# Performance work log

Hardware: AMD Instinct MI355X
Metric: run time of the kernel (lower is better)

Reference implementation:

```python
import jax, jax.numpy as jnp
import numpy as np

N, E = 4096, 4096          # nodes, hyperedges
IN_DIM, OUT_DIM, EDGE_DIM = 256, 256, 64
HEADS, DEG, CARD = 8, 8, 8  # node degree, edge cardinality (regular hypergraph)


def setup_inputs() -> dict:
    key = jax.random.key(0)
    ks = jax.random.split(key, 6)
    # regular hypergraph: DEG rounds, each a permutation of nodes chunked into
    # blocks of CARD -> every node in exactly DEG edges, every edge has CARD
    # distinct nodes. E = DEG * N / CARD.
    rng = np.random.default_rng(0)
    node_of_edge = np.concatenate(
        [rng.permutation(N).reshape(-1, CARD) for _ in range(DEG)], axis=0)  # [E, CARD]
    inc = np.zeros((E, N), dtype=np.float32)
    inc[np.arange(E)[:, None], node_of_edge] = 1.0
    s = 0.05
    return {
        "x": jax.random.normal(ks[0], (N, IN_DIM), jnp.float32),
        "incidence": jnp.asarray(inc),
        "edge_attr": jax.random.normal(ks[1], (E, EDGE_DIM), jnp.float32),
        "W_lin": jax.random.normal(ks[2], (IN_DIM, OUT_DIM), jnp.float32) * s,
        "W_edge": jax.random.normal(ks[3], (EDGE_DIM, OUT_DIM), jnp.float32) * s,
        "in_proj_w": jax.random.normal(ks[4], (3 * OUT_DIM, OUT_DIM), jnp.float32) * s,
        "in_proj_b": jnp.zeros((3 * OUT_DIM,), jnp.float32),
        "out_proj_w": jax.random.normal(ks[5], (OUT_DIM, OUT_DIM), jnp.float32) * s,
        "out_proj_b": jnp.zeros((OUT_DIM,), jnp.float32),
        "deg": DEG,
        "card": CARD,
    }


def reference(x, incidence, edge_attr, W_lin, W_edge,
              in_proj_w, in_proj_b, out_proj_w, out_proj_b, deg, card):
    n = x.shape[0]
    Wh = x @ W_lin          # [N, D]
    We = edge_attr @ W_edge  # [E, D]
    Dm = Wh.shape[1]
    H = HEADS
    dh = Dm // H
    # recover regular structure from the binary incidence matrix.
    # (attention is permutation-invariant over the pair set, so the order of
    #  indices returned by top_k vs torch.nonzero does not matter)
    _, edge_of_node = jax.lax.top_k(incidence.T, deg)   # [N, deg]
    _, node_of_edge = jax.lax.top_k(incidence, card)    # [E, card]
    pair_e = edge_of_node[:, :, None]                   # [N, deg, 1]
    pair_u = node_of_edge[edge_of_node]                 # [N, deg, card]
    L = deg * card
    Ksrc = (Wh[pair_u] + We[pair_e]).reshape(n, L, Dm)  # key source per pair
    Vsrc = Wh[pair_u].reshape(n, L, Dm)                 # value source per pair
    # torch nn.MultiheadAttention in/out projections
    Wq, Wk, Wv = jnp.split(in_proj_w, 3, axis=0)
    bq, bk, bv = jnp.split(in_proj_b, 3)
    q = (Wh @ Wq.T + bq).reshape(n, H, dh)              # q_len = 1 per node
    k = (Ksrc @ Wk.T + bk).reshape(n, L, H, dh)
    v = (Vsrc @ Wv.T + bv).reshape(n, L, H, dh)
    scale = 1.0 / jnp.sqrt(jnp.asarray(dh, q.dtype))
    scores = jnp.einsum('nhd,nlhd->nhl', q, k) * scale  # [N, H, L]
    attn = jax.nn.softmax(scores, axis=-1)
    ctx = jnp.einsum('nhl,nlhd->nhd', attn, v).reshape(n, Dm)
    out = ctx @ out_proj_w.T + out_proj_b
    return jax.nn.relu(out)
```

## Files before the change

kernel.cpp:

```cpp
#include <hip/hip_runtime.h>
#include <hip/hip_bf16.h>

#define NN    4096
#define EE    4096
#define DM    256
#define EDIM  64
#define HH    8
#define DHd   32
#define LL    64

typedef short  s16x8 __attribute__((ext_vector_type(8)));
typedef unsigned short u16x8 __attribute__((ext_vector_type(8)));
typedef float  f32x4 __attribute__((ext_vector_type(4)));

#define SCALE 0.17677669529663687f

__device__ __forceinline__ float b2f(unsigned short u) {
  return __uint_as_float(((unsigned int)u) << 16);
}
__device__ __forceinline__ unsigned short f2b_bits(float f) {
  unsigned int u = __float_as_uint(f);
  u = (u + 0x7FFFu + ((u >> 16) & 1u)) >> 16;
  return (unsigned short)u;
}

#define MODE_PLAIN 0
#define MODE_PROJ  1
#define MODE_OUT   2

__device__ __forceinline__ void gemm_mfma_body(
    short* As, short* Bs, f32x4 acc[2][2], int wr, int wc, int fr, int fk) {
  s16x8 af0 = *(const s16x8*)&As[(wr + fr) * 40 + fk];
  s16x8 af1 = *(const s16x8*)&As[(wr + 16 + fr) * 40 + fk];
  s16x8 bf0 = *(const s16x8*)&Bs[(wc + fr) * 40 + fk];
  s16x8 bf1 = *(const s16x8*)&Bs[(wc + 16 + fr) * 40 + fk];
  acc[0][0] = __builtin_amdgcn_mfma_f32_16x16x32_bf16(af0, bf0, acc[0][0], 0, 0, 0);
  acc[0][1] = __builtin_amdgcn_mfma_f32_16x16x32_bf16(af0, bf1, acc[0][1], 0, 0, 0);
  acc[1][0] = __builtin_amdgcn_mfma_f32_16x16x32_bf16(af1, bf0, acc[1][0], 0, 0, 0);
  acc[1][1] = __builtin_amdgcn_mfma_f32_16x16x32_bf16(af1, bf1, acc[1][1], 0, 0, 0);
}

__device__ __forceinline__ void gemm_tile(
    const unsigned short* __restrict__ A, const unsigned short* __restrict__ B,
    int i0, int j0, int N, int K, int mode,
    float* __restrict__ out_f, unsigned short* __restrict__ out_b,
    unsigned short* __restrict__ out_b2, const float* __restrict__ bias,
    short* As, short* Bs) {
  const int tid  = threadIdx.x;
  const int wid  = tid >> 6, lane = tid & 63;
  const int wr   = (wid >> 1) * 32, wc = (wid & 1) * 32;
  const int srow = tid >> 2, schunk = (tid & 3) * 8;
  const int fr   = lane & 15, fk = (lane >> 4) * 8;

  f32x4 acc[2][2];
#pragma unroll
  for (int a = 0; a < 2; ++a)
#pragma unroll
    for (int b = 0; b < 2; ++b) acc[a][b] = (f32x4){0.f, 0.f, 0.f, 0.f};

  for (int kk = 0; kk < K; kk += 32) {
    *(s16x8*)&As[srow * 40 + schunk] = *(const s16x8*)&A[(size_t)(i0 + srow) * K + kk + schunk];
    *(s16x8*)&Bs[srow * 40 + schunk] = *(const s16x8*)&B[(size_t)(j0 + srow) * K + kk + schunk];
    __syncthreads();
    gemm_mfma_body(As, Bs, acc, wr, wc, fr, fk);
    __syncthreads();
  }

  const int ecol = lane & 15, erow0 = (lane >> 4) * 4;
#pragma unroll
  for (int mi = 0; mi < 2; ++mi)
#pragma unroll
    for (int ni = 0; ni < 2; ++ni) {
#pragma unroll
      for (int v = 0; v < 4; ++v) {
        int i = i0 + wr + mi * 16 + erow0 + v;
        int j = j0 + wc + ni * 16 + ecol;
        float val = acc[mi][ni][v];
        if (mode == MODE_PLAIN) {
          out_b[(size_t)i * N + j] = f2b_bits(val);
        } else if (mode == MODE_PROJ) {
          if (j < 256)      out_b[(size_t)i * 256 + j]           = f2b_bits((val + bias[j]) * SCALE);
          else if (j < 512) out_b2[(size_t)i * 256 + (j - 256)]  = f2b_bits(val);
          else              ((unsigned short*)out_f)[(size_t)i * 256 + (j - 512)] = f2b_bits(val + bias[j]);
        } else {
          float r = val + bias[j];
          out_f[(size_t)i * N + j] = r > 0.f ? r : 0.f;
        }
      }
    }
}

__device__ __forceinline__ void gemm_tile_f32src(
    const float* __restrict__ A, const float* __restrict__ B,
    int i0, int j0, int N, int K,
    unsigned short* __restrict__ out_b, short* As, short* Bs) {
  const int tid  = threadIdx.x;
  const int wid  = tid >> 6, lane = tid & 63;
  const int wr   = (wid >> 1) * 32, wc = (wid & 1) * 32;
  const int srow = tid >> 2, schunk = (tid & 3) * 8;
  const int fr   = lane & 15, fk = (lane >> 4) * 8;

  f32x4 acc[2][2];
#pragma unroll
  for (int a = 0; a < 2; ++a)
#pragma unroll
    for (int b = 0; b < 2; ++b) acc[a][b] = (f32x4){0.f, 0.f, 0.f, 0.f};

  for (int kk = 0; kk < K; kk += 32) {
    float4 a0 = *(const float4*)&A[(size_t)(i0 + srow) * K + kk + schunk];
    float4 a1 = *(const float4*)&A[(size_t)(i0 + srow) * K + kk + schunk + 4];
    float4 b0 = *(const float4*)&B[(size_t)(j0 + srow) * K + kk + schunk];
    float4 b1 = *(const float4*)&B[(size_t)(j0 + srow) * K + kk + schunk + 4];
    s16x8 av, bv;
    av[0] = (short)f2b_bits(a0.x); av[1] = (short)f2b_bits(a0.y);
    av[2] = (short)f2b_bits(a0.z); av[3] = (short)f2b_bits(a0.w);
    av[4] = (short)f2b_bits(a1.x); av[5] = (short)f2b_bits(a1.y);
    av[6] = (short)f2b_bits(a1.z); av[7] = (short)f2b_bits(a1.w);
    bv[0] = (short)f2b_bits(b0.x); bv[1] = (short)f2b_bits(b0.y);
    bv[2] = (short)f2b_bits(b0.z); bv[3] = (short)f2b_bits(b0.w);
    bv[4] = (short)f2b_bits(b1.x); bv[5] = (short)f2b_bits(b1.y);
    bv[6] = (short)f2b_bits(b1.z); bv[7] = (short)f2b_bits(b1.w);
    *(s16x8*)&As[srow * 40 + schunk] = av;
    *(s16x8*)&Bs[srow * 40 + schunk] = bv;
    __syncthreads();
    gemm_mfma_body(As, Bs, acc, wr, wc, fr, fk);
    __syncthreads();
  }

  const int ecol = lane & 15, erow0 = (lane >> 4) * 4;
#pragma unroll
  for (int mi = 0; mi < 2; ++mi)
#pragma unroll
    for (int ni = 0; ni < 2; ++ni)
#pragma unroll
      for (int v = 0; v < 4; ++v) {
        int i = i0 + wr + mi * 16 + erow0 + v;
        int j = j0 + wc + ni * 16 + ecol;
        if (j < N) out_b[(size_t)i * N + j] = f2b_bits(acc[mi][ni][v]);
      }
}

__global__ __launch_bounds__(256) void mega1(
    const float* __restrict__ inc,
    int* __restrict__ cnt_e, int* __restrict__ cnt_n,
    int* __restrict__ noe, int* __restrict__ eon,
    const float* __restrict__ x, const float* __restrict__ ea,
    const float* __restrict__ wout,
    unsigned short* __restrict__ xb, unsigned short* __restrict__ eab,
    unsigned short* __restrict__ woutb,
    const float* __restrict__ ipw, const float* __restrict__ wlin,
    const float* __restrict__ wedge,
    unsigned short* __restrict__ F, unsigned short* __restrict__ G) {
  __shared__ short As[64 * 40] __attribute__((aligned(16)));
  __shared__ short Bs[64 * 40] __attribute__((aligned(16)));
  const int bid = blockIdx.x;
  if (bid < 16384) {
    int t = bid * 256 + threadIdx.x;
    float4 v = ((const float4*)inc)[t];
    int flat = t * 4;
    int e  = flat >> 12;
    int u0 = flat & 4095;
    float vals[4] = {v.x, v.y, v.z, v.w};
#pragma unroll
    for (int j = 0; j < 4; ++j) {
      if (vals[j] != 0.0f) {
        int u  = u0 + j;
        int pe = atomicAdd(&cnt_e[e], 1);
        noe[e * 8 + pe] = u;
        int pn = atomicAdd(&cnt_n[u], 1);
        eon[u * 8 + pn] = e;
      }
    }
    return;
  }
  if (bid < 17728) {
    int j = (bid - 16384) * 256 + threadIdx.x;
    const float* src; unsigned short* dst;
    if (j < 262144)      { src = x;    dst = xb; }
    else { j -= 262144;
    if (j < 65536)       { src = ea;   dst = eab; }
    else { j -= 65536;     src = wout; dst = woutb; } }
    float4 v = ((const float4*)src)[j];
    ushort4 o;
    o.x = f2b_bits(v.x); o.y = f2b_bits(v.y); o.z = f2b_bits(v.z); o.w = f2b_bits(v.w);
    ((ushort4*)dst)[j] = o;
    return;
  }
  int fb = bid - 17728;
  if (fb < 48) {
    gemm_tile_f32src(ipw, wlin, (fb >> 2) * 64, (fb & 3) * 64, 256, 256, F, As, Bs);
  } else {
    gemm_tile_f32src(ipw + 65536, wedge, (fb - 48) * 64, 0, 64, 256, G, As, Bs);
  }
}

__global__ __launch_bounds__(256) void mega2(
    const unsigned short* __restrict__ x_bf, const unsigned short* __restrict__ F,
    const unsigned short* __restrict__ ea_bf, const unsigned short* __restrict__ G,
    unsigned short* __restrict__ Q, unsigned short* __restrict__ Kn,
    unsigned short* __restrict__ Vn, unsigned short* __restrict__ Ke,
    const float* __restrict__ ipb,
    const int* __restrict__ eon, const int* __restrict__ noe,
    int* __restrict__ pair_u) {
  __shared__ short As[64 * 40] __attribute__((aligned(16)));
  __shared__ short Bs[64 * 40] __attribute__((aligned(16)));
  const int bid = blockIdx.x;
  if (bid < 768) {
    gemm_tile(x_bf, F, (bid & 63) * 64, (bid >> 6) * 64, 768, 256,
              MODE_PROJ, (float*)Vn, Q, Kn, ipb, As, Bs);
  } else if (bid < 1024) {
    int r = bid - 768;
    gemm_tile(ea_bf, G, (r & 63) * 64, (r >> 6) * 64, 256, 64,
              MODE_PLAIN, nullptr, Ke, nullptr, nullptr, As, Bs);
  } else {
    int wv = ((bid - 1024) * 256 + threadIdx.x) >> 6;
    int lane = threadIdx.x & 63;
#pragma unroll
    for (int r = 0; r < 16; ++r) {
      int n = wv * 16 + r;
      int e = eon[n * 8 + (lane >> 3)];
      pair_u[n * 64 + lane] = noe[e * 8 + (lane & 7)];
    }
  }
}

__global__ __launch_bounds__(256) void attn_kernel(
    const unsigned short* __restrict__ Q, const unsigned short* __restrict__ Kn,
    const unsigned short* __restrict__ Vn, const unsigned short* __restrict__ Ke,
    const int* __restrict__ eon, const int* __restrict__ pair_u,
    unsigned short* __restrict__ ctx) {
  const int w = (blockIdx.x * 256 + threadIdx.x) >> 6;
  const int n = w >> 3, h = w & 7;
  const int lane = threadIdx.x & 63;
  const int rg = lane & 15, dchunk = lane >> 4;

  const int u = pair_u[n * 64 + lane];
  const int e = eon[n * 8 + (lane >> 3)];

  int ur[4];
#pragma unroll
  for (int i = 0; i < 4; ++i) ur[i] = __shfl(u, rg * 4 + i, 64);
  u16x8 vstage[4];
#pragma unroll
  for (int i = 0; i < 4; ++i)
    vstage[i] = *(const u16x8*)(Vn + (size_t)ur[i] * 256 + h * 32 + dchunk * 8);

  const u16x8* kp = (const u16x8*)(Kn + (size_t)u * 256 + h * 32);
  const u16x8* ep = (const u16x8*)(Ke + (size_t)e * 256 + h * 32);
  const u16x8* qp = (const u16x8*)(Q  + (size_t)n * 256 + h * 32);
  float s = 0.f;
#pragma unroll
  for (int c = 0; c < 4; ++c) {
    u16x8 kv = kp[c], ev = ep[c], qv = qp[c];
#pragma unroll
    for (int j = 0; j < 8; ++j)
      s += b2f(qv[j]) * (b2f(kv[j]) + b2f(ev[j]));
  }

  float m = s;
#pragma unroll
  for (int off = 32; off >= 1; off >>= 1) m = fmaxf(m, __shfl_xor(m, off));
  float p = __expf(s - m);
  float sum = p;
#pragma unroll
  for (int off = 32; off >= 1; off >>= 1) sum += __shfl_xor(sum, off);
  const float a = __fdividef(p, sum);

  float acc[8];
#pragma unroll
  for (int j = 0; j < 8; ++j) acc[j] = 0.f;
#pragma unroll
  for (int i = 0; i < 4; ++i) {
    float pi = __shfl(a, rg * 4 + i, 64);
#pragma unroll
    for (int j = 0; j < 8; ++j) acc[j] += pi * b2f(vstage[i][j]);
  }
#pragma unroll
  for (int off = 1; off < 16; off <<= 1)
#pragma unroll
    for (int j = 0; j < 8; ++j) acc[j] += __shfl_xor(acc[j], off, 64);

  if (rg == 0) {
    u16x8 o;
#pragma unroll
    for (int j = 0; j < 8; ++j) o[j] = f2b_bits(acc[j]);
    *(u16x8*)(ctx + (size_t)n * 256 + h * 32 + dchunk * 8) = o;
  }
}

__global__ __launch_bounds__(256) void gemm_out(
    const unsigned short* __restrict__ ctx, const unsigned short* __restrict__ wout_bf,
    float* __restrict__ out, const float* __restrict__ bias) {
  __shared__ short As[64 * 40] __attribute__((aligned(16)));
  __shared__ short Bs[64 * 40] __attribute__((aligned(16)));
  gemm_tile(ctx, wout_bf, blockIdx.x * 64, blockIdx.y * 64, 256, 256,
            MODE_OUT, out, nullptr, nullptr, bias, As, Bs);
}

#define MB_ ((size_t)1048576)
#define OFF_Q      ((size_t)0)
#define OFF_KN     (2*MB_)
#define OFF_VN     (4*MB_)
#define OFF_KE     (6*MB_)
#define OFF_CTX    (8*MB_)
#define OFF_XBF    (10*MB_)
#define OFF_EABF   (12*MB_)
#define OFF_WOUTBF (12*MB_+524288)
#define OFF_F      (13*MB_)
#define OFF_G      (13*MB_+524288)
#define OFF_PAIRU  (14*MB_)
#define OFF_CNTE   (15*MB_)
#define OFF_CNTN   (15*MB_+16384)
#define OFF_NOE    (15*MB_+32768)
#define OFF_EON    (15*MB_+163840)

extern "C" void kernel_launch(void* const* d_in, const int* in_sizes, int n_in,
                              void* d_out, int out_size, void* d_ws, size_t ws_size,
                              hipStream_t stream) {
  const float* x     = (const float*)d_in[0];
  const float* inc   = (const float*)d_in[1];
  const float* ea    = (const float*)d_in[2];
  const float* wlin  = (const float*)d_in[3];
  const float* wedge = (const float*)d_in[4];
  const float* ipw   = (const float*)d_in[5];
  const float* ipb   = (const float*)d_in[6];
  const float* wout  = (const float*)d_in[7];
  const float* outb  = (const float*)d_in[8];

  char* ws = (char*)d_ws;
  unsigned short* Q       = (unsigned short*)(ws + OFF_Q);
  unsigned short* Kn      = (unsigned short*)(ws + OFF_KN);
  unsigned short* Vn      = (unsigned short*)(ws + OFF_VN);
  unsigned short* Ke      = (unsigned short*)(ws + OFF_KE);
  unsigned short* ctx     = (unsigned short*)(ws + OFF_CTX);
  unsigned short* x_bf    = (unsigned short*)(ws + OFF_XBF);
  unsigned short* ea_bf   = (unsigned short*)(ws + OFF_EABF);
  unsigned short* wout_bf = (unsigned short*)(ws + OFF_WOUTBF);
  unsigned short* F       = (unsigned short*)(ws + OFF_F);
  unsigned short* G       = (unsigned short*)(ws + OFF_G);
  int*            cnt_e   = (int*)(ws + OFF_CNTE);
  int*            noe     = (int*)(ws + OFF_NOE);
  int*            eon     = (int*)(ws + OFF_EON);
  int*            pair_u  = (int*)(ws + OFF_PAIRU);

  hipMemsetAsync(ws + OFF_CNTE, 0, 32768, stream);

  mega1<<<17780, 256, 0, stream>>>(inc, cnt_e, (int*)(ws + OFF_CNTN), noe, eon,
                                   x, ea, wout, x_bf, ea_bf, wout_bf,
                                   ipw, wlin, wedge, F, G);
  mega2<<<1088, 256, 0, stream>>>(x_bf, F, ea_bf, G, Q, Kn, Vn, Ke, ipb,
                                  eon, noe, pair_u);
  attn_kernel<<<8192, 256, 0, stream>>>(Q, Kn, Vn, Ke, eon, pair_u, ctx);
  gemm_out<<<dim3(64, 4), 256, 0, stream>>>(ctx, wout_bf, (float*)d_out, outb);
}
```

Measured before the change: 92.20 us.

## Stage per-node K and edge rows in swizzled LDS, one block per node

```diff
diff --git a/kernel.cpp b/kernel.cpp
--- a/kernel.cpp
+++ b/kernel.cpp
@@ -224,34 +224,60 @@
   }
 }
 
-__global__ __launch_bounds__(256) void attn_kernel(
+__global__ __launch_bounds__(512) void attn_kernel(
     const unsigned short* __restrict__ Q, const unsigned short* __restrict__ Kn,
     const unsigned short* __restrict__ Vn, const unsigned short* __restrict__ Ke,
     const int* __restrict__ eon, const int* __restrict__ pair_u,
     unsigned short* __restrict__ ctx) {
-  const int w = (blockIdx.x * 256 + threadIdx.x) >> 6;
-  const int n = w >> 3, h = w & 7;
-  const int lane = threadIdx.x & 63;
+  const int n = blockIdx.x;
+  __shared__ unsigned short Klds[64 * 256] __attribute__((aligned(16)));
+  __shared__ unsigned short Elds[8 * 256]  __attribute__((aligned(16)));
+  const int tid = threadIdx.x;
+  const int h = tid >> 6, lane = tid & 63;
   const int rg = lane & 15, dchunk = lane >> 4;
 
-  const int u = pair_u[n * 64 + lane];
-  const int e = eon[n * 8 + (lane >> 3)];
-
+  {
+    const int w = h;
+#pragma unroll
+    for (int j = 0; j < 4; ++j) {
+      int row = w * 8 + j * 2 + (lane >> 5);
+      int u   = pair_u[n * 64 + row];
+      u16x8 v = *(const u16x8*)(Kn + (size_t)u * 256 + (lane & 31) * 8);
+      int db  = (row * 512 + (lane & 31) * 16) ^ ((row & 7) << 4);
+      *(u16x8*)((char*)Klds + db) = v;
+    }
+    if (tid < 64) {
+#pragma unroll
+      for (int j = 0; j < 4; ++j) {
+        int row = j * 2 + (tid >> 5);
+        int e   = eon[n * 8 + row];
+        u16x8 v = *(const u16x8*)(Ke + (size_t)e * 256 + (tid & 31) * 8);
+        int db  = (row * 512 + (tid & 31) * 16) ^ ((row & 7) << 4);
+        *(u16x8*)((char*)Elds + db) = v;
+      }
+    }
+  }
+
+  const int ul = pair_u[n * 64 + lane];
   int ur[4];
 #pragma unroll
-  for (int i = 0; i < 4; ++i) ur[i] = __shfl(u, rg * 4 + i, 64);
+  for (int i = 0; i < 4; ++i) ur[i] = __shfl(ul, rg * 4 + i, 64);
   u16x8 vstage[4];
 #pragma unroll
   for (int i = 0; i < 4; ++i)
     vstage[i] = *(const u16x8*)(Vn + (size_t)ur[i] * 256 + h * 32 + dchunk * 8);
 
-  const u16x8* kp = (const u16x8*)(Kn + (size_t)u * 256 + h * 32);
-  const u16x8* ep = (const u16x8*)(Ke + (size_t)e * 256 + h * 32);
-  const u16x8* qp = (const u16x8*)(Q  + (size_t)n * 256 + h * 32);
+  __syncthreads();
+
+  const u16x8* qp = (const u16x8*)(Q + (size_t)n * 256 + h * 32);
+  const int kbase = lane * 512 + h * 64, ksw = (lane & 7) << 4;
+  const int ebase = (lane >> 3) * 512 + h * 64, esw = ((lane >> 3) & 7) << 4;
   float s = 0.f;
 #pragma unroll
   for (int c = 0; c < 4; ++c) {
-    u16x8 kv = kp[c], ev = ep[c], qv = qp[c];
+    u16x8 kv = *(const u16x8*)((const char*)Klds + ((kbase + c * 16) ^ ksw));
+    u16x8 ev = *(const u16x8*)((const char*)Elds + ((ebase + c * 16) ^ esw));
+    u16x8 qv = qp[c];
 #pragma unroll
     for (int j = 0; j < 8; ++j)
       s += b2f(qv[j]) * (b2f(kv[j]) + b2f(ev[j]));
@@ -350,6 +376,6 @@
                                    ipw, wlin, wedge, F, G);
   mega2<<<1088, 256, 0, stream>>>(x_bf, F, ea_bf, G, Q, Kn, Vn, Ke, ipb,
                                   eon, noe, pair_u);
-  attn_kernel<<<8192, 256, 0, stream>>>(Q, Kn, Vn, Ke, eon, pair_u, ctx);
+  attn_kernel<<<4096, 512, 0, stream>>>(Q, Kn, Vn, Ke, eon, pair_u, ctx);
   gemm_out<<<dim3(64, 4), 256, 0, stream>>>(ctx, wout_bf, (float*)d_out, outb);
 }
```

After: 93.34 us. Within noise of the previous version (+1.2%).
